# Kernel tuning notes

Hardware: AMD Instinct MI355X
Metric: run time of the kernel (lower is better)

Reference implementation:

```python
import jax, jax.numpy as jnp
import numpy as np

B, T, C = 4, 2048, 1024
H, D = 16, 64

def setup_inputs() -> dict:
    key = jax.random.key(0)
    k1, k2, k3 = jax.random.split(key, 3)
    x = jax.random.normal(k1, (B, T, C), dtype=jnp.float32)
    Wqkv = jax.random.normal(k2, (C, 3 * C), dtype=jnp.float32) * (1.0 / np.sqrt(C))
    Wproj = jax.random.normal(k3, (C, C), dtype=jnp.float32) * (1.0 / np.sqrt(C))
    return {"x": x, "Wqkv": Wqkv, "Wproj": Wproj}

def reference(x, Wqkv, Wproj):
    Bx, Tx, Cx = x.shape
    qkv = x @ Wqkv                       # (B, T, 3C)
    q, k, v = jnp.split(qkv, 3, axis=-1)
    # (B, T, C) -> (B, H, T, D)
    q = q.reshape(Bx, Tx, H, D).transpose(0, 2, 1, 3)
    k = k.reshape(Bx, Tx, H, D).transpose(0, 2, 1, 3)
    v = v.reshape(Bx, Tx, H, D).transpose(0, 2, 1, 3)
    att = jnp.einsum('bhqd,bhkd->bhqk', q, k) / jnp.sqrt(jnp.float32(D))
    causal = jnp.tril(jnp.ones((Tx, Tx), dtype=bool))  # (T, T)
    att = jnp.where(causal[None, None, :, :], att, jnp.float32(-jnp.inf))
    att = jax.nn.softmax(att, axis=-1)
    y = jnp.einsum('bhqk,bhkd->bhqd', att, v)          # (B, H, T, D)
    y = y.transpose(0, 2, 1, 3).reshape(Bx, Tx, Cx)
    return y @ Wproj
```

## Files before the change

kernel.cpp:

```cpp
#include <hip/hip_runtime.h>
#include <cstdint>
#include <cstddef>


typedef short bf16x8 __attribute__((ext_vector_type(8)));
typedef float f32x4 __attribute__((ext_vector_type(4)));

#define MFMA32(a, b, c) __builtin_amdgcn_mfma_f32_16x16x32_bf16((a), (b), (c), 0, 0, 0)

__device__ __forceinline__ unsigned short f2b(float f) {
  unsigned int x = __builtin_bit_cast(unsigned int, f);
  x += 0x7fffu + ((x >> 16) & 1u);
  return (unsigned short)(x >> 16);
}

__device__ __forceinline__ unsigned int pack2(float a, float b) {
  return (unsigned int)f2b(a) | ((unsigned int)f2b(b) << 16);
}

__device__ __forceinline__ void gload16(const void* g, void* l) {
  __builtin_amdgcn_global_load_lds(
      (const __attribute__((address_space(1))) void*)g,
      (__attribute__((address_space(3))) void*)l, 16, 0, 0);
}

__global__ __launch_bounds__(256) void k_conv_x(const float* __restrict__ in,
                                                unsigned short* __restrict__ out, int n4) {
  int i = blockIdx.x * 256 + threadIdx.x;
  if (i >= n4) return;
  float4 v = reinterpret_cast<const float4*>(in)[i];
  ushort4 o;
  o.x = f2b(v.x); o.y = f2b(v.y); o.z = f2b(v.z); o.w = f2b(v.w);
  reinterpret_cast<ushort4*>(out)[i] = o;
}

__global__ __launch_bounds__(256) void k_transpose(const float* __restrict__ in,
                                                   unsigned short* __restrict__ out,
                                                   int R, int C) {
  __shared__ float tile[32][33];
  int c0 = blockIdx.x * 32, r0 = blockIdx.y * 32;
  int tx = threadIdx.x & 31, ty = threadIdx.x >> 5;
#pragma unroll
  for (int j = 0; j < 4; ++j)
    tile[ty + 8 * j][tx] = in[(size_t)(r0 + ty + 8 * j) * C + c0 + tx];
  __syncthreads();
#pragma unroll
  for (int j = 0; j < 4; ++j)
    out[(size_t)(c0 + ty + 8 * j) * R + r0 + tx] = f2b(tile[tx][ty + 8 * j]);
}

template <int EPI>
__global__ __launch_bounds__(256) void k_gemm(const unsigned short* __restrict__ A,
                                              const unsigned short* __restrict__ Bt,
                                              float* __restrict__ outF,
                                              unsigned short* __restrict__ q_ws,
                                              unsigned short* __restrict__ k_ws,
                                              unsigned short* __restrict__ v_ws,
                                              int M, int N) {
  constexpr int K = 1024;
  __shared__ unsigned short As[128 * 64];
  __shared__ unsigned short Bs[128 * 64];
  const int bn = blockIdx.x, bm = blockIdx.y;
  const int tid = threadIdx.x;
  const int w = tid >> 6, lane = tid & 63;
  const int wm = w >> 1, wn = w & 1;
  const int c = lane & 15, g = lane >> 4;

  f32x4 acc[4][4];
#pragma unroll
  for (int i = 0; i < 4; ++i)
#pragma unroll
    for (int j = 0; j < 4; ++j) acc[i][j] = (f32x4){0.f, 0.f, 0.f, 0.f};

  const int srow = 32 * w + (lane >> 3);
  const int scol = 8 * (lane & 7);
  const unsigned short* Ag = A + (size_t)(bm * 128 + srow) * K + scol;
  const unsigned short* Bg = Bt + (size_t)(bn * 128 + srow) * K + scol;
  char* AsB = (char*)As + w * 4096;
  char* BsB = (char*)Bs + w * 4096;

  for (int kt = 0; kt < K / 64; ++kt) {
    const int kb = kt * 64;
    __syncthreads();
#pragma unroll
    for (int i = 0; i < 4; ++i) {
      gload16(Ag + (size_t)(8 * i) * K + kb, AsB + i * 1024);
      gload16(Bg + (size_t)(8 * i) * K + kb, BsB + i * 1024);
    }
    asm volatile("s_waitcnt vmcnt(0)" ::: "memory");
    __syncthreads();
#pragma unroll
    for (int u = 0; u < 2; ++u) {
      bf16x8 af[4], bfr[4];
#pragma unroll
      for (int mf = 0; mf < 4; ++mf)
        af[mf] = *(const bf16x8*)((const char*)As + (wm * 64 + mf * 16 + c) * 128 + u * 64 + g * 16);
#pragma unroll
      for (int nf = 0; nf < 4; ++nf)
        bfr[nf] = *(const bf16x8*)((const char*)Bs + (wn * 64 + nf * 16 + c) * 128 + u * 64 + g * 16);
#pragma unroll
      for (int mf = 0; mf < 4; ++mf)
#pragma unroll
        for (int nf = 0; nf < 4; ++nf)
          acc[mf][nf] = MFMA32(af[mf], bfr[nf], acc[mf][nf]);
    }
  }

  const int rowb = bm * 128 + wm * 64;
  const int colb = bn * 128 + wn * 64;
  if (EPI == 1) {
#pragma unroll
    for (int mf = 0; mf < 4; ++mf)
#pragma unroll
      for (int nf = 0; nf < 4; ++nf)
#pragma unroll
        for (int r = 0; r < 4; ++r) {
          int row = rowb + mf * 16 + 4 * g + r;
          int col = colb + nf * 16 + c;
          outF[(size_t)row * N + col] = acc[mf][nf][r];
        }
  } else {
#pragma unroll
    for (int mf = 0; mf < 4; ++mf)
#pragma unroll
      for (int nf = 0; nf < 4; ++nf)
#pragma unroll
        for (int r = 0; r < 4; ++r) {
          int row = rowb + mf * 16 + 4 * g + r;
          int col = colb + nf * 16 + c;
          int sec = col >> 10, cc = col & 1023;
          int h = cc >> 6, d = cc & 63;
          int b = row >> 11, t = row & 2047;
          float v = acc[mf][nf][r];
          if (sec == 0) {
            q_ws[((size_t)(b * 16 + h) * 2048 + t) * 64 + d] = f2b(v * 0.125f);
          } else if (sec == 1) {
            int dsw = ((((d >> 3) ^ (t & 7)) & 7) << 3) | (d & 7);
            k_ws[((size_t)(b * 16 + h) * 2048 + t) * 64 + dsw] = f2b(v);
          } else {
            int tsw = (t & ~63) | (((((t >> 3) & 7) ^ (d & 7)) & 7) << 3) | (t & 7);
            v_ws[((size_t)(b * 16 + h) * 64 + d) * 2048 + tsw] = f2b(v);
          }
        }
  }
}

__global__ __launch_bounds__(512) void k_attn(const unsigned short* __restrict__ q_ws,
                                              const unsigned short* __restrict__ k_ws,
                                              const unsigned short* __restrict__ v_ws,
                                              unsigned short* __restrict__ y_ws) {
  constexpr int T = 2048;
  __shared__ unsigned short Ks[64 * 64];
  __shared__ unsigned short Vs[64 * 64];
  const int f = blockIdx.x;
  const int f2 = (f & 7) * 64 + (f >> 3);
  const int bh = f2 >> 3;
  const int xi = f2 & 7;
  const int tid = threadIdx.x, w = tid >> 6, lane = tid & 63;
  const int c = lane & 15, g = lane >> 4;
  const int cl = c & 7;
  const size_t base = (size_t)bh * T * 64;
  const unsigned short* Kb = k_ws + base;
  const unsigned short* Vb = v_ws + base;
  const unsigned short* Qb = q_ws + base;

  const int s_row = w * 8 + (lane >> 3);
  const int s_ch = lane & 7;
  char* KsW = (char*)Ks + w * 1024;
  char* VsW = (char*)Vs + w * 1024;

#pragma unroll 1
  for (int ph = 0; ph < 2; ++ph) {
    const int q0 = (ph == 0 ? xi : 15 - xi) * 128;
    const int qrow = q0 + 16 * w + c;
    const int q_max_wave = q0 + 16 * w + 15;
    bf16x8 qf[2];
#pragma unroll
    for (int u = 0; u < 2; ++u)
      qf[u] = *(const bf16x8*)(Qb + (size_t)qrow * 64 + 32 * u + 8 * g);

    f32x4 yacc[4];
#pragma unroll
    for (int i = 0; i < 4; ++i) yacc[i] = (f32x4){0.f, 0.f, 0.f, 0.f};
    float m_run = -1e30f, l_part = 0.f;
    const int n_kt = (q0 >> 6) + 2;

#pragma unroll 1
    for (int kt = 0; kt < n_kt; ++kt) {
      const int k0 = kt * 64;
      __syncthreads();
      gload16(Kb + (size_t)(k0 + s_row) * 64 + s_ch * 8, KsW);
      gload16(Vb + (size_t)s_row * T + k0 + s_ch * 8, VsW);
      asm volatile("s_waitcnt vmcnt(0)" ::: "memory");
      __syncthreads();
      if (k0 > q_max_wave) continue;

      f32x4 s[4];
#pragma unroll
      for (int tf = 0; tf < 4; ++tf) {
        bf16x8 kf0 = *(const bf16x8*)((const char*)Ks + (16 * tf + c) * 128 + ((g) ^ cl) * 16);
        bf16x8 kf1 = *(const bf16x8*)((const char*)Ks + (16 * tf + c) * 128 + ((4 + g) ^ cl) * 16);
        f32x4 z = (f32x4){0.f, 0.f, 0.f, 0.f};
        z = MFMA32(kf0, qf[0], z);
        s[tf] = MFMA32(kf1, qf[1], z);
      }
      if (k0 + 63 > q0 + 16 * w) {
#pragma unroll
        for (int tf = 0; tf < 4; ++tf)
#pragma unroll
          for (int r = 0; r < 4; ++r)
            if (k0 + 16 * tf + 4 * g + r > qrow) s[tf][r] = -1e30f;
      }
      float mx0 = fmaxf(fmaxf(s[0][0], s[0][1]), fmaxf(s[0][2], s[0][3]));
      float mx1 = fmaxf(fmaxf(s[1][0], s[1][1]), fmaxf(s[1][2], s[1][3]));
      float mx2 = fmaxf(fmaxf(s[2][0], s[2][1]), fmaxf(s[2][2], s[2][3]));
      float mx3 = fmaxf(fmaxf(s[3][0], s[3][1]), fmaxf(s[3][2], s[3][3]));
      float mx = fmaxf(fmaxf(mx0, mx1), fmaxf(mx2, mx3));
      mx = fmaxf(mx, __shfl_xor(mx, 16));
      mx = fmaxf(mx, __shfl_xor(mx, 32));
      if (__any(mx > m_run + 8.f)) {
        float m_new = fmaxf(m_run, mx);
        float corr = __expf(m_run - m_new);
        l_part *= corr;
#pragma unroll
        for (int i = 0; i < 4; ++i) yacc[i] *= corr;
        m_run = m_new;
      }
      float p[16];
#pragma unroll
      for (int tf = 0; tf < 4; ++tf)
#pragma unroll
        for (int r = 0; r < 4; ++r) p[tf * 4 + r] = __expf(s[tf][r] - m_run);
      float ps = ((p[0] + p[1]) + (p[2] + p[3])) + ((p[4] + p[5]) + (p[6] + p[7]));
      ps += ((p[8] + p[9]) + (p[10] + p[11])) + ((p[12] + p[13]) + (p[14] + p[15]));
      l_part += ps;

#pragma unroll
      for (int h = 0; h < 2; ++h) {
        unsigned int lo0 = pack2(p[8 * h + 0], p[8 * h + 1]);
        unsigned int hi0 = pack2(p[8 * h + 2], p[8 * h + 3]);
        unsigned int lo1 = pack2(p[8 * h + 4], p[8 * h + 5]);
        unsigned int hi1 = pack2(p[8 * h + 6], p[8 * h + 7]);
        int a2 = 2 * (g & 1);
        int srcA = 16 * a2 + c, srcB = srcA + 16;
        unsigned int Al0 = __shfl(lo0, srcA), Ah0 = __shfl(hi0, srcA);
        unsigned int Al1 = __shfl(lo1, srcA), Ah1 = __shfl(hi1, srcA);
        unsigned int Bl0 = __shfl(lo0, srcB), Bh0 = __shfl(hi0, srcB);
        unsigned int Bl1 = __shfl(lo1, srcB), Bh1 = __shfl(hi1, srcB);
        bool f1 = (g >= 2);
        union { unsigned int u[4]; bf16x8 v; } pf;
        pf.u[0] = f1 ? Al1 : Al0;
        pf.u[1] = f1 ? Ah1 : Ah0;
        pf.u[2] = f1 ? Bl1 : Bl0;
        pf.u[3] = f1 ? Bh1 : Bh0;
#pragma unroll
        for (int df = 0; df < 4; ++df) {
          bf16x8 vf = *(const bf16x8*)((const char*)Vs + (16 * df + c) * 128 + ((h * 4 + g) ^ cl) * 16);
          yacc[df] = MFMA32(vf, pf.v, yacc[df]);
        }
      }
    }

    float lt = l_part;
    lt += __shfl_xor(lt, 16);
    lt += __shfl_xor(lt, 32);
    float inv = 1.f / lt;
    const int b = bh >> 4, hh = bh & 15;
#pragma unroll
    for (int df = 0; df < 4; ++df) {
      uint2 o;
      o.x = pack2(yacc[df][0] * inv, yacc[df][1] * inv);
      o.y = pack2(yacc[df][2] * inv, yacc[df][3] * inv);
      *(uint2*)(y_ws + (size_t)(b * 2048 + qrow) * 1024 + hh * 64 + 16 * df + 4 * g) = o;
    }
  }
}

extern "C" void kernel_launch(void* const* d_in, const int* in_sizes, int n_in,
                              void* d_out, int out_size, void* d_ws, size_t ws_size,
                              hipStream_t stream) {
  const float* x = (const float*)d_in[0];
  const float* Wqkv = (const float*)d_in[1];
  const float* Wproj = (const float*)d_in[2];
  float* out = (float*)d_out;
  char* ws = (char*)d_ws;

  unsigned short* x_bf = (unsigned short*)(ws);
  unsigned short* wqkvT = (unsigned short*)(ws + 16777216);
  unsigned short* wprojT = (unsigned short*)(ws + 23068672);
  unsigned short* q_ws = (unsigned short*)(ws + 25165824);
  unsigned short* k_ws = (unsigned short*)(ws + 41943040);
  unsigned short* v_ws = (unsigned short*)(ws + 58720256);
  unsigned short* y_ws = (unsigned short*)(ws + 75497472);

  k_conv_x<<<8192, 256, 0, stream>>>(x, x_bf, 2097152);
  k_transpose<<<dim3(96, 32), 256, 0, stream>>>(Wqkv, wqkvT, 1024, 3072);
  k_transpose<<<dim3(32, 32), 256, 0, stream>>>(Wproj, wprojT, 1024, 1024);
  k_gemm<0><<<dim3(24, 64), 256, 0, stream>>>(x_bf, wqkvT, nullptr, q_ws, k_ws, v_ws, 8192, 3072);
  k_attn<<<512, 512, 0, stream>>>(q_ws, k_ws, v_ws, y_ws);
  k_gemm<1><<<dim3(8, 64), 256, 0, stream>>>(y_ws, wprojT, out, nullptr, nullptr, nullptr, 8192, 1024);
}
```

Before: 201.8 us.

## Double-buffer K/V tiles in attention, use 64-row Q blocks and exp2 softmax

The attention kernel now prefetches the next K/V tile into a second LDS buffer while the current tile is computed, replacing the load-then-wait pattern. Blocks shrink to 4 waves covering 64 query rows, and twice as many blocks are launched, which cuts wasted causal tiles per block. The softmax moves to base-2 exponentials by folding log2(e) into the Q scale and calling v_exp_f32 directly, and P is packed to bf16 with the hardware v_cvt_pk_bf16_f32 instruction. The rescale threshold is raised to match the base-2 domain. The risks are doubled LDS per block and an extra barrier per iteration.

```diff
diff --git a/kernel.cpp b/kernel.cpp
--- a/kernel.cpp
+++ b/kernel.cpp
@@ -16,6 +16,18 @@
 
 __device__ __forceinline__ unsigned int pack2(float a, float b) {
   return (unsigned int)f2b(a) | ((unsigned int)f2b(b) << 16);
+}
+
+__device__ __forceinline__ unsigned int cvtpk(float a, float b) {
+  unsigned int r;
+  asm("v_cvt_pk_bf16_f32 %0, %1, %2" : "=v"(r) : "v"(a), "v"(b));
+  return r;
+}
+
+__device__ __forceinline__ float exp2v(float x) {
+  float r;
+  asm("v_exp_f32 %0, %1" : "=v"(r) : "v"(x));
+  return r;
 }
 
 __device__ __forceinline__ void gload16(const void* g, void* l) {
@@ -120,6 +132,7 @@
           outF[(size_t)row * N + col] = acc[mf][nf][r];
         }
   } else {
+    const float QSC = 0.125f * 1.4426950408889634f;
 #pragma unroll
     for (int mf = 0; mf < 4; ++mf)
 #pragma unroll
@@ -133,7 +146,7 @@
           int b = row >> 11, t = row & 2047;
           float v = acc[mf][nf][r];
           if (sec == 0) {
-            q_ws[((size_t)(b * 16 + h) * 2048 + t) * 64 + d] = f2b(v * 0.125f);
+            q_ws[((size_t)(b * 16 + h) * 2048 + t) * 64 + d] = f2b(v * QSC);
           } else if (sec == 1) {
             int dsw = ((((d >> 3) ^ (t & 7)) & 7) << 3) | (d & 7);
             k_ws[((size_t)(b * 16 + h) * 2048 + t) * 64 + dsw] = f2b(v);
@@ -145,17 +158,17 @@
   }
 }
 
-__global__ __launch_bounds__(512) void k_attn(const unsigned short* __restrict__ q_ws,
+__global__ __launch_bounds__(256) void k_attn(const unsigned short* __restrict__ q_ws,
                                               const unsigned short* __restrict__ k_ws,
                                               const unsigned short* __restrict__ v_ws,
                                               unsigned short* __restrict__ y_ws) {
   constexpr int T = 2048;
-  __shared__ unsigned short Ks[64 * 64];
-  __shared__ unsigned short Vs[64 * 64];
+  __shared__ unsigned short Ks[2][64 * 64];
+  __shared__ unsigned short Vs[2][64 * 64];
   const int f = blockIdx.x;
-  const int f2 = (f & 7) * 64 + (f >> 3);
-  const int bh = f2 >> 3;
-  const int xi = f2 & 7;
+  const int f2 = (f & 7) * 128 + (f >> 3);
+  const int bh = f2 >> 4;
+  const int xi = f2 & 15;
   const int tid = threadIdx.x, w = tid >> 6, lane = tid & 63;
   const int c = lane & 15, g = lane >> 4;
   const int cl = c & 7;
@@ -164,16 +177,15 @@
   const unsigned short* Vb = v_ws + base;
   const unsigned short* Qb = q_ws + base;
 
-  const int s_row = w * 8 + (lane >> 3);
-  const int s_ch = lane & 7;
-  char* KsW = (char*)Ks + w * 1024;
-  char* VsW = (char*)Vs + w * 1024;
+  const int srow = 16 * w + (lane >> 3);
+  const int sch = lane & 7;
 
 #pragma unroll 1
   for (int ph = 0; ph < 2; ++ph) {
-    const int q0 = (ph == 0 ? xi : 15 - xi) * 128;
+    const int q0 = (ph == 0 ? xi : 31 - xi) * 64;
     const int qrow = q0 + 16 * w + c;
     const int q_max_wave = q0 + 16 * w + 15;
+    const int n_kt = (q0 >> 6) + 1;
     bf16x8 qf[2];
 #pragma unroll
     for (int u = 0; u < 2; ++u)
@@ -183,82 +195,105 @@
 #pragma unroll
     for (int i = 0; i < 4; ++i) yacc[i] = (f32x4){0.f, 0.f, 0.f, 0.f};
     float m_run = -1e30f, l_part = 0.f;
-    const int n_kt = (q0 >> 6) + 2;
+    int cur = 0;
+
+    __syncthreads();
+    {
+      char* KsW = (char*)&Ks[0][0] + w * 2048;
+      char* VsW = (char*)&Vs[0][0] + w * 2048;
+      gload16(Kb + (size_t)srow * 64 + sch * 8, KsW);
+      gload16(Kb + (size_t)(srow + 8) * 64 + sch * 8, KsW + 1024);
+      gload16(Vb + (size_t)srow * T + sch * 8, VsW);
+      gload16(Vb + (size_t)(srow + 8) * T + sch * 8, VsW + 1024);
+    }
 
 #pragma unroll 1
     for (int kt = 0; kt < n_kt; ++kt) {
       const int k0 = kt * 64;
+      if (kt + 1 < n_kt) {
+        const int k0n = k0 + 64;
+        char* KsW = (char*)&Ks[cur ^ 1][0] + w * 2048;
+        char* VsW = (char*)&Vs[cur ^ 1][0] + w * 2048;
+        gload16(Kb + (size_t)(k0n + srow) * 64 + sch * 8, KsW);
+        gload16(Kb + (size_t)(k0n + srow + 8) * 64 + sch * 8, KsW + 1024);
+        gload16(Vb + (size_t)srow * T + k0n + sch * 8, VsW);
+        gload16(Vb + (size_t)(srow + 8) * T + k0n + sch * 8, VsW + 1024);
+        asm volatile("s_waitcnt vmcnt(4)" ::: "memory");
+      } else {
+        asm volatile("s_waitcnt vmcnt(0)" ::: "memory");
+      }
       __syncthreads();
-      gload16(Kb + (size_t)(k0 + s_row) * 64 + s_ch * 8, KsW);
-      gload16(Vb + (size_t)s_row * T + k0 + s_ch * 8, VsW);
-      asm volatile("s_waitcnt vmcnt(0)" ::: "memory");
+
+      if (k0 <= q_max_wave) {
+        const char* KsC = (const char*)&Ks[cur][0];
+        const char* VsC = (const char*)&Vs[cur][0];
+        f32x4 s[4];
+#pragma unroll
+        for (int tf = 0; tf < 4; ++tf) {
+          bf16x8 kf0 = *(const bf16x8*)(KsC + (16 * tf + c) * 128 + (g ^ cl) * 16);
+          bf16x8 kf1 = *(const bf16x8*)(KsC + (16 * tf + c) * 128 + ((4 + g) ^ cl) * 16);
+          f32x4 z = (f32x4){0.f, 0.f, 0.f, 0.f};
+          z = MFMA32(kf0, qf[0], z);
+          s[tf] = MFMA32(kf1, qf[1], z);
+        }
+        if (k0 + 63 > q0 + 16 * w) {
+#pragma unroll
+          for (int tf = 0; tf < 4; ++tf)
+#pragma unroll
+            for (int r = 0; r < 4; ++r)
+              if (k0 + 16 * tf + 4 * g + r > qrow) s[tf][r] = -1e30f;
+        }
+        float mx0 = fmaxf(fmaxf(s[0][0], s[0][1]), fmaxf(s[0][2], s[0][3]));
+        float mx1 = fmaxf(fmaxf(s[1][0], s[1][1]), fmaxf(s[1][2], s[1][3]));
+        float mx2 = fmaxf(fmaxf(s[2][0], s[2][1]), fmaxf(s[2][2], s[2][3]));
+        float mx3 = fmaxf(fmaxf(s[3][0], s[3][1]), fmaxf(s[3][2], s[3][3]));
+        float mx = fmaxf(fmaxf(mx0, mx1), fmaxf(mx2, mx3));
+        mx = fmaxf(mx, __shfl_xor(mx, 16));
+        mx = fmaxf(mx, __shfl_xor(mx, 32));
+        if (__any(mx > m_run + 11.5f)) {
+          float m_new = fmaxf(m_run, mx);
+          float corr = exp2v(m_run - m_new);
+          l_part *= corr;
+#pragma unroll
+          for (int i = 0; i < 4; ++i) yacc[i] *= corr;
+          m_run = m_new;
+        }
+        float p[16];
+#pragma unroll
+        for (int tf = 0; tf < 4; ++tf)
+#pragma unroll
+          for (int r = 0; r < 4; ++r) p[tf * 4 + r] = exp2v(s[tf][r] - m_run);
+        float ps = ((p[0] + p[1]) + (p[2] + p[3])) + ((p[4] + p[5]) + (p[6] + p[7]));
+        ps += ((p[8] + p[9]) + (p[10] + p[11])) + ((p[12] + p[13]) + (p[14] + p[15]));
+        l_part += ps;
+
+#pragma unroll
+        for (int h = 0; h < 2; ++h) {
+          unsigned int lo0 = cvtpk(p[8 * h + 0], p[8 * h + 1]);
+          unsigned int hi0 = cvtpk(p[8 * h + 2], p[8 * h + 3]);
+          unsigned int lo1 = cvtpk(p[8 * h + 4], p[8 * h + 5]);
+          unsigned int hi1 = cvtpk(p[8 * h + 6], p[8 * h + 7]);
+          int a2 = 2 * (g & 1);
+          int srcA = 16 * a2 + c, srcB = srcA + 16;
+          unsigned int Al0 = __shfl(lo0, srcA), Ah0 = __shfl(hi0, srcA);
+          unsigned int Al1 = __shfl(lo1, srcA), Ah1 = __shfl(hi1, srcA);
+          unsigned int Bl0 = __shfl(lo0, srcB), Bh0 = __shfl(hi0, srcB);
+          unsigned int Bl1 = __shfl(lo1, srcB), Bh1 = __shfl(hi1, srcB);
+          bool f1 = (g >= 2);
+          union { unsigned int u[4]; bf16x8 v; } pf;
+          pf.u[0] = f1 ? Al1 : Al0;
+          pf.u[1] = f1 ? Ah1 : Ah0;
+          pf.u[2] = f1 ? Bl1 : Bl0;
+          pf.u[3] = f1 ? Bh1 : Bh0;
+#pragma unroll
+          for (int df = 0; df < 4; ++df) {
+            bf16x8 vf = *(const bf16x8*)(VsC + (16 * df + c) * 128 + ((h * 4 + g) ^ cl) * 16);
+            yacc[df] = MFMA32(vf, pf.v, yacc[df]);
+          }
+        }
+      }
       __syncthreads();
-      if (k0 > q_max_wave) continue;
-
-      f32x4 s[4];
-#pragma unroll
-      for (int tf = 0; tf < 4; ++tf) {
-        bf16x8 kf0 = *(const bf16x8*)((const char*)Ks + (16 * tf + c) * 128 + ((g) ^ cl) * 16);
-        bf16x8 kf1 = *(const bf16x8*)((const char*)Ks + (16 * tf + c) * 128 + ((4 + g) ^ cl) * 16);
-        f32x4 z = (f32x4){0.f, 0.f, 0.f, 0.f};
-        z = MFMA32(kf0, qf[0], z);
-        s[tf] = MFMA32(kf1, qf[1], z);
-      }
-      if (k0 + 63 > q0 + 16 * w) {
-#pragma unroll
-        for (int tf = 0; tf < 4; ++tf)
-#pragma unroll
-          for (int r = 0; r < 4; ++r)
-            if (k0 + 16 * tf + 4 * g + r > qrow) s[tf][r] = -1e30f;
-      }
-      float mx0 = fmaxf(fmaxf(s[0][0], s[0][1]), fmaxf(s[0][2], s[0][3]));
-      float mx1 = fmaxf(fmaxf(s[1][0], s[1][1]), fmaxf(s[1][2], s[1][3]));
-      float mx2 = fmaxf(fmaxf(s[2][0], s[2][1]), fmaxf(s[2][2], s[2][3]));
-      float mx3 = fmaxf(fmaxf(s[3][0], s[3][1]), fmaxf(s[3][2], s[3][3]));
-      float mx = fmaxf(fmaxf(mx0, mx1), fmaxf(mx2, mx3));
-      mx = fmaxf(mx, __shfl_xor(mx, 16));
-      mx = fmaxf(mx, __shfl_xor(mx, 32));
-      if (__any(mx > m_run + 8.f)) {
-        float m_new = fmaxf(m_run, mx);
-        float corr = __expf(m_run - m_new);
-        l_part *= corr;
-#pragma unroll
-        for (int i = 0; i < 4; ++i) yacc[i] *= corr;
-        m_run = m_new;
-      }
-      float p[16];
-#pragma unroll
-      for (int tf = 0; tf < 4; ++tf)
-#pragma unroll
-        for (int r = 0; r < 4; ++r) p[tf * 4 + r] = __expf(s[tf][r] - m_run);
-      float ps = ((p[0] + p[1]) + (p[2] + p[3])) + ((p[4] + p[5]) + (p[6] + p[7]));
-      ps += ((p[8] + p[9]) + (p[10] + p[11])) + ((p[12] + p[13]) + (p[14] + p[15]));
-      l_part += ps;
-
-#pragma unroll
-      for (int h = 0; h < 2; ++h) {
-        unsigned int lo0 = pack2(p[8 * h + 0], p[8 * h + 1]);
-        unsigned int hi0 = pack2(p[8 * h + 2], p[8 * h + 3]);
-        unsigned int lo1 = pack2(p[8 * h + 4], p[8 * h + 5]);
-        unsigned int hi1 = pack2(p[8 * h + 6], p[8 * h + 7]);
-        int a2 = 2 * (g & 1);
-        int srcA = 16 * a2 + c, srcB = srcA + 16;
-        unsigned int Al0 = __shfl(lo0, srcA), Ah0 = __shfl(hi0, srcA);
-        unsigned int Al1 = __shfl(lo1, srcA), Ah1 = __shfl(hi1, srcA);
-        unsigned int Bl0 = __shfl(lo0, srcB), Bh0 = __shfl(hi0, srcB);
-        unsigned int Bl1 = __shfl(lo1, srcB), Bh1 = __shfl(hi1, srcB);
-        bool f1 = (g >= 2);
-        union { unsigned int u[4]; bf16x8 v; } pf;
-        pf.u[0] = f1 ? Al1 : Al0;
-        pf.u[1] = f1 ? Ah1 : Ah0;
-        pf.u[2] = f1 ? Bl1 : Bl0;
-        pf.u[3] = f1 ? Bh1 : Bh0;
-#pragma unroll
-        for (int df = 0; df < 4; ++df) {
-          bf16x8 vf = *(const bf16x8*)((const char*)Vs + (16 * df + c) * 128 + ((h * 4 + g) ^ cl) * 16);
-          yacc[df] = MFMA32(vf, pf.v, yacc[df]);
-        }
-      }
+      cur ^= 1;
     }
 
     float lt = l_part;
@@ -297,6 +332,6 @@
   k_transpose<<<dim3(96, 32), 256, 0, stream>>>(Wqkv, wqkvT, 1024, 3072);
   k_transpose<<<dim3(32, 32), 256, 0, stream>>>(Wproj, wprojT, 1024, 1024);
   k_gemm<0><<<dim3(24, 64), 256, 0, stream>>>(x_bf, wqkvT, nullptr, q_ws, k_ws, v_ws, 8192, 3072);
-  k_attn<<<512, 512, 0, stream>>>(q_ws, k_ws, v_ws, y_ws);
+  k_attn<<<1024, 256, 0, stream>>>(q_ws, k_ws, v_ws, y_ws);
   k_gemm<1><<<dim3(8, 64), 256, 0, stream>>>(y_ws, wprojT, out, nullptr, nullptr, nullptr, 8192, 1024);
 }
```

Result: slower. 221.5 us (+9.8%).
